# Kernel optimization log

Hardware: AMD Instinct MI355X
Metric: run time of the kernel (lower is better)

## Reference

```python
import jax, jax.numpy as jnp
import numpy as np

N_NODES = 100000
N_EDGES = 640000
D_IN = 128
D_H = 128


def setup_inputs() -> dict:
    key = jax.random.key(0)
    ks = jax.random.split(key, 24)
    def W(k, shp):
        return jax.random.normal(k, shp, dtype=jnp.float32) * 0.05
    inp = {
        "x": jax.random.normal(ks[0], (N_NODES, D_IN), dtype=jnp.float32),
        "src": jax.random.randint(ks[1], (N_EDGES,), 0, N_NODES, dtype=jnp.int32),
        "dst": jax.random.randint(ks[2], (N_EDGES,), 0, N_NODES, dtype=jnp.int32),
        "neg_src": jax.random.randint(ks[3], (N_EDGES,), 0, N_NODES, dtype=jnp.int32),
        "neg_dst": jax.random.randint(ks[4], (N_EDGES,), 0, N_NODES, dtype=jnp.int32),
        # SAGEConv layer 1/2/3: fc_self weight, fc_neigh weight (stored [in,out]), bias
        "Ws1": W(ks[5], (D_IN, D_H)), "Wn1": W(ks[6], (D_IN, D_H)), "b1": jnp.zeros((D_H,), jnp.float32),
        "Ws2": W(ks[7], (D_H, D_H)), "Wn2": W(ks[8], (D_H, D_H)), "b2": jnp.zeros((D_H,), jnp.float32),
        "Ws3": W(ks[9], (D_H, D_H)), "Wn3": W(ks[10], (D_H, D_H)), "b3": jnp.zeros((D_H,), jnp.float32),
        # MLPPredictor: W1 [2h,h], W2 [h,1]
        "Wp1": W(ks[11], (2 * D_H, D_H)), "bp1": jnp.zeros((D_H,), jnp.float32),
        "Wp2": W(ks[12], (D_H, 1)), "bp2": jnp.zeros((1,), jnp.float32),
    }
    return inp


def _sage_mean(x, src, dst, Ws, Wn, b):
    # DGL SAGEConv 'mean': rst = fc_self(h) + fc_neigh(mean_{in-neighbors}(h)) + bias
    n = x.shape[0]
    msum = jax.ops.segment_sum(x[src], dst, num_segments=n)        # [N, d]
    deg = jax.ops.segment_sum(jnp.ones_like(src, dtype=x.dtype), dst, num_segments=n)
    mean = msum / jnp.clip(deg, 1.0)[:, None]                      # zero for isolated nodes
    return x @ Ws + mean @ Wn + b


def _edge_score(h, s, d, Wp1, bp1, Wp2, bp2):
    z = jnp.concatenate([h[s], h[d]], axis=1)                      # [E, 2h]
    return (jax.nn.relu(z @ Wp1 + bp1) @ Wp2 + bp2)[:, 0]          # [E]


def reference(x, src, dst, neg_src, neg_dst,
              Ws1, Wn1, b1, Ws2, Wn2, b2, Ws3, Wn3, b3,
              Wp1, bp1, Wp2, bp2):
    h = _sage_mean(x, src, dst, Ws1, Wn1, b1)
    h = _sage_mean(h, src, dst, Ws2, Wn2, b2)
    h = _sage_mean(h, src, dst, Ws3, Wn3, b3)
    pos = _edge_score(h, src, dst, Wp1, bp1, Wp2, bp2)
    neg = _edge_score(h, neg_src, neg_dst, Wp1, bp1, Wp2, bp2)
    return (pos, neg)
```

## Files before the change

kernel.cpp:

```cpp
#include <hip/hip_runtime.h>

#define N_NODES 100000
#define N_EDGES 640000
#define D 128
#define SCAN_TILE 1024
#define SCAN_BLOCKS ((N_NODES + SCAN_TILE - 1) / SCAN_TILE)

typedef __attribute__((ext_vector_type(8))) short bf16x8;
typedef __attribute__((ext_vector_type(4))) float f32x4;

__device__ __forceinline__ unsigned short f32_to_bf16(float f) {
  union { float f; unsigned int u; } v; v.f = f;
  unsigned int u = v.u;
  unsigned int r = (u + 0x7fffu + ((u >> 16) & 1u)) >> 16;
  return (unsigned short)r;
}
__device__ __forceinline__ float bf16_lo(unsigned int u) { return __uint_as_float(u << 16); }
__device__ __forceinline__ float bf16_hi(unsigned int u) { return __uint_as_float(u & 0xffff0000u); }

__device__ __forceinline__ void acc8(float* a, uint4 r) {
  a[0] += bf16_lo(r.x); a[1] += bf16_hi(r.x);
  a[2] += bf16_lo(r.y); a[3] += bf16_hi(r.y);
  a[4] += bf16_lo(r.z); a[5] += bf16_hi(r.z);
  a[6] += bf16_lo(r.w); a[7] += bf16_hi(r.w);
}

__global__ void zero_i32(int* __restrict__ p, int n) {
  int i = blockIdx.x * blockDim.x + threadIdx.x;
  if (i < n) p[i] = 0;
}

__global__ void f32_to_bf16_vec(const float* __restrict__ in, unsigned short* __restrict__ out, int n4) {
  int i = blockIdx.x * blockDim.x + threadIdx.x;
  if (i < n4) {
    float4 v = ((const float4*)in)[i];
    ushort4 o;
    o.x = f32_to_bf16(v.x); o.y = f32_to_bf16(v.y);
    o.z = f32_to_bf16(v.z); o.w = f32_to_bf16(v.w);
    ((ushort4*)out)[i] = o;
  }
}

__global__ void transpose_w(const float* __restrict__ W0, const float* __restrict__ W1,
                            const float* __restrict__ W2, const float* __restrict__ W3,
                            const float* __restrict__ W4, const float* __restrict__ W5,
                            const float* __restrict__ W6, const float* __restrict__ W7,
                            unsigned short* __restrict__ wt) {
  int id = blockIdx.x * 256 + threadIdx.x;
  int mat = id >> 14;
  int rem = id & 16383;
  int n = rem >> 7, k = rem & 127;
  const float* Wm = mat < 4 ? (mat < 2 ? (mat == 0 ? W0 : W1) : (mat == 2 ? W2 : W3))
                            : (mat < 6 ? (mat == 4 ? W4 : W5) : (mat == 6 ? W6 : W7));
  wt[id] = f32_to_bf16(Wm[k * D + n]);
}

__global__ void hist_kernel(const int* __restrict__ dst, int* __restrict__ deg, int E) {
  int i = blockIdx.x * blockDim.x + threadIdx.x;
  if (i < E) atomicAdd(&deg[dst[i]], 1);
}

__global__ void scan_blocksum(const int* __restrict__ deg, int* __restrict__ partial, int n) {
  __shared__ int lds[256];
  const int tid = threadIdx.x;
  const int base = blockIdx.x * SCAN_TILE + tid * 4;
  int s = 0;
#pragma unroll
  for (int j = 0; j < 4; ++j) {
    int i = base + j;
    if (i < n) s += deg[i];
  }
  lds[tid] = s;
  __syncthreads();
  for (int off = 128; off > 0; off >>= 1) {
    if (tid < off) lds[tid] += lds[tid + off];
    __syncthreads();
  }
  if (tid == 0) partial[blockIdx.x] = lds[0];
}

__global__ void scan_offsets(int* __restrict__ partial, int* __restrict__ row_start, int nb, int n) {
  __shared__ int lds[128];
  const int tid = threadIdx.x;
  int v = (tid < nb) ? partial[tid] : 0;
  lds[tid] = v;
  __syncthreads();
  for (int off = 1; off < 128; off <<= 1) {
    int t = (tid >= off) ? lds[tid - off] : 0;
    __syncthreads();
    lds[tid] += t;
    __syncthreads();
  }
  if (tid < nb) partial[tid] = (tid == 0) ? 0 : lds[tid - 1];
  if (tid == 0) row_start[n] = lds[nb - 1];
}

__global__ void scan_final(const int* __restrict__ deg, const int* __restrict__ partial,
                           int* __restrict__ row_start, int n) {
  __shared__ int lds[256];
  const int tid = threadIdx.x;
  const int base = blockIdx.x * SCAN_TILE + tid * 4;
  int d[4];
  int s = 0;
#pragma unroll
  for (int j = 0; j < 4; ++j) {
    int i = base + j;
    d[j] = (i < n) ? deg[i] : 0;
    s += d[j];
  }
  lds[tid] = s;
  __syncthreads();
  for (int off = 1; off < 256; off <<= 1) {
    int t = (tid >= off) ? lds[tid - off] : 0;
    __syncthreads();
    lds[tid] += t;
    __syncthreads();
  }
  int pre = partial[blockIdx.x] + lds[tid] - s;
#pragma unroll
  for (int j = 0; j < 4; ++j) {
    int i = base + j;
    if (i < n) {
      row_start[i] = pre;
      pre += d[j];
    }
  }
}

__global__ void fill_kernel(const int* __restrict__ src, const int* __restrict__ dst,
                            const int* __restrict__ row_start, int* __restrict__ cursor,
                            int* __restrict__ esrc, int E) {
  int i = blockIdx.x * blockDim.x + threadIdx.x;
  if (i < E) {
    int d = dst[i];
    int pos = atomicAdd(&cursor[d], 1);
    esrc[row_start[d] + pos] = src[i];
  }
}

__global__ __launch_bounds__(256) void gather_mean(
    const unsigned short* __restrict__ hin,
    const int* __restrict__ row_start, const int* __restrict__ esrc,
    unsigned short* __restrict__ mean, int M) {
  const int t = blockIdx.x * blockDim.x + threadIdx.x;
  const int node = t >> 4;
  const int fl = t & 15;
  if (node >= M) return;
  const int s0 = row_start[node], s1 = row_start[node + 1];
  float ac[8] = {0.f, 0.f, 0.f, 0.f, 0.f, 0.f, 0.f, 0.f};
  int e = s0;
  for (; e + 4 <= s1; e += 4) {
    int i0 = esrc[e], i1 = esrc[e + 1], i2 = esrc[e + 2], i3 = esrc[e + 3];
    uint4 r0 = *(const uint4*)(hin + (((size_t)i0) << 7) + fl * 8);
    uint4 r1 = *(const uint4*)(hin + (((size_t)i1) << 7) + fl * 8);
    uint4 r2 = *(const uint4*)(hin + (((size_t)i2) << 7) + fl * 8);
    uint4 r3 = *(const uint4*)(hin + (((size_t)i3) << 7) + fl * 8);
    acc8(ac, r0); acc8(ac, r1); acc8(ac, r2); acc8(ac, r3);
  }
  for (; e < s1; ++e) {
    uint4 r0 = *(const uint4*)(hin + (((size_t)esrc[e]) << 7) + fl * 8);
    acc8(ac, r0);
  }
  const float inv = 1.0f / (float)max(s1 - s0, 1);
#pragma unroll
  for (int k = 0; k < 8; ++k) ac[k] *= inv;
  uint4 o;
  o.x = (unsigned)f32_to_bf16(ac[0]) | ((unsigned)f32_to_bf16(ac[1]) << 16);
  o.y = (unsigned)f32_to_bf16(ac[2]) | ((unsigned)f32_to_bf16(ac[3]) << 16);
  o.z = (unsigned)f32_to_bf16(ac[4]) | ((unsigned)f32_to_bf16(ac[5]) << 16);
  o.w = (unsigned)f32_to_bf16(ac[6]) | ((unsigned)f32_to_bf16(ac[7]) << 16);
  *reinterpret_cast<uint4*>(mean + (((size_t)node) << 7) + fl * 8) = o;
}

template <bool PRED>
__global__ __launch_bounds__(256) void layer_mlp(
    const unsigned short* __restrict__ hin,
    const unsigned short* __restrict__ mean,
    const unsigned short* __restrict__ Wts, const unsigned short* __restrict__ Wtn,
    const float* __restrict__ bias,
    const unsigned short* __restrict__ WtA, const unsigned short* __restrict__ WtB,
    const float* __restrict__ biasA,
    unsigned short* __restrict__ out0, unsigned short* __restrict__ out1, int M) {
  __shared__ unsigned short wl[64][136];
  const int tid = threadIdx.x;
  const int lane = tid & 63;
  const int wave = tid >> 6;
  const int m0 = blockIdx.x * 128;
  const int row = lane & 15;
  const int q = lane >> 4;
  const int mloadA = min(m0 + wave * 16 + row, M - 1);
  const int mloadB = min(m0 + 64 + wave * 16 + row, M - 1);
  const int lrow = wave * 16 + row;

  auto stage64 = [&](const unsigned short* W, int half) {
#pragma unroll
    for (int i = 0; i < 4; ++i) {
      int seg = i * 256 + tid;
      int r = seg >> 4, o = (seg & 15) * 8;
      *reinterpret_cast<bf16x8*>(&wl[r][o]) =
          *reinterpret_cast<const bf16x8*>(W + (size_t)(half * 64 + r) * D + o);
    }
  };
  auto mfma_half = [&](bf16x8* a, f32x4* accp) {
#pragma unroll
    for (int s = 0; s < 4; ++s)
#pragma unroll
      for (int t = 0; t < 4; ++t) {
        bf16x8 b = *reinterpret_cast<const bf16x8*>(&wl[t * 16 + row][s * 32 + q * 8]);
        accp[t] = __builtin_amdgcn_mfma_f32_16x16x32_bf16(a[s], b, accp[t], 0, 0, 0);
      }
  };
  auto epilogue = [&](f32x4* accp, const float* bvec, unsigned short* dst, int base) {
    __syncthreads();
#pragma unroll
    for (int t = 0; t < 8; ++t) {
      const int col = t * 16 + row;
      const float bv = bvec ? bvec[col] : 0.f;
#pragma unroll
      for (int r = 0; r < 4; ++r)
        wl[wave * 16 + q * 4 + r][col] = f32_to_bf16(accp[t][r] + bv);
    }
    __syncthreads();
#pragma unroll
    for (int i = 0; i < 4; ++i) {
      int idx = i * 256 + tid;
      int r2 = idx >> 4;
      int c8 = (idx & 15) * 8;
      int m = base + r2;
      if (m < M)
        *reinterpret_cast<uint4*>(dst + (size_t)m * D + c8) =
            *reinterpret_cast<const uint4*>(&wl[r2][c8]);
    }
  };

  stage64(Wts, 0);
  bf16x8 ahA[4], amA[4], ahB[4], amB[4];
#pragma unroll
  for (int s = 0; s < 4; ++s) {
    ahA[s] = *reinterpret_cast<const bf16x8*>(hin + (size_t)mloadA * D + s * 32 + q * 8);
    amA[s] = *reinterpret_cast<const bf16x8*>(mean + (size_t)mloadA * D + s * 32 + q * 8);
    ahB[s] = *reinterpret_cast<const bf16x8*>(hin + (size_t)mloadB * D + s * 32 + q * 8);
    amB[s] = *reinterpret_cast<const bf16x8*>(mean + (size_t)mloadB * D + s * 32 + q * 8);
  }
  __syncthreads();

  f32x4 accA[8], accB[8];
#pragma unroll
  for (int t = 0; t < 8; ++t) { accA[t] = (f32x4){0.f, 0.f, 0.f, 0.f}; accB[t] = (f32x4){0.f, 0.f, 0.f, 0.f}; }

  mfma_half(ahA, accA); mfma_half(ahB, accB);
  __syncthreads(); stage64(Wts, 1); __syncthreads();
  mfma_half(ahA, accA + 4); mfma_half(ahB, accB + 4);
  __syncthreads(); stage64(Wtn, 0); __syncthreads();
  mfma_half(amA, accA); mfma_half(amB, accB);
  __syncthreads(); stage64(Wtn, 1); __syncthreads();
  mfma_half(amA, accA + 4); mfma_half(amB, accB + 4);

  if (!PRED) {
    epilogue(accA, bias, out0, m0);
    epilogue(accB, bias, out0, m0 + 64);
    return;
  }

  __syncthreads();
  bf16x8 apA[4], apB[4];
#pragma unroll
  for (int t = 0; t < 8; ++t) {
    const int col = t * 16 + row;
    const float bv = bias[col];
#pragma unroll
    for (int r = 0; r < 4; ++r)
      wl[wave * 16 + q * 4 + r][col] = f32_to_bf16(accA[t][r] + bv);
  }
#pragma unroll
  for (int s = 0; s < 4; ++s)
    apA[s] = *reinterpret_cast<const bf16x8*>(&wl[lrow][s * 32 + q * 8]);
#pragma unroll
  for (int t = 0; t < 8; ++t) {
    const int col = t * 16 + row;
    const float bv = bias[col];
#pragma unroll
    for (int r = 0; r < 4; ++r)
      wl[wave * 16 + q * 4 + r][col] = f32_to_bf16(accB[t][r] + bv);
  }
#pragma unroll
  for (int s = 0; s < 4; ++s)
    apB[s] = *reinterpret_cast<const bf16x8*>(&wl[lrow][s * 32 + q * 8]);
  __syncthreads();

  stage64(WtA, 0);
  __syncthreads();
#pragma unroll
  for (int t = 0; t < 8; ++t) { accA[t] = (f32x4){0.f, 0.f, 0.f, 0.f}; accB[t] = (f32x4){0.f, 0.f, 0.f, 0.f}; }
  mfma_half(apA, accA); mfma_half(apB, accB);
  __syncthreads(); stage64(WtA, 1); __syncthreads();
  mfma_half(apA, accA + 4); mfma_half(apB, accB + 4);
  epilogue(accA, biasA, out0, m0);
  epilogue(accB, biasA, out0, m0 + 64);
  __syncthreads();
  stage64(WtB, 0);
  __syncthreads();
#pragma unroll
  for (int t = 0; t < 8; ++t) { accA[t] = (f32x4){0.f, 0.f, 0.f, 0.f}; accB[t] = (f32x4){0.f, 0.f, 0.f, 0.f}; }
  mfma_half(apA, accA); mfma_half(apB, accB);
  __syncthreads(); stage64(WtB, 1); __syncthreads();
  mfma_half(apA, accA + 4); mfma_half(apB, accB + 4);
  epilogue(accA, nullptr, out1, m0);
  epilogue(accB, nullptr, out1, m0 + 64);
}

__device__ __forceinline__ float relu_dot8(uint4 a, uint4 b, float4 w0, float4 w1) {
  return fmaxf(bf16_lo(a.x) + bf16_lo(b.x), 0.f) * w0.x +
         fmaxf(bf16_hi(a.x) + bf16_hi(b.x), 0.f) * w0.y +
         fmaxf(bf16_lo(a.y) + bf16_lo(b.y), 0.f) * w0.z +
         fmaxf(bf16_hi(a.y) + bf16_hi(b.y), 0.f) * w0.w +
         fmaxf(bf16_lo(a.z) + bf16_lo(b.z), 0.f) * w1.x +
         fmaxf(bf16_hi(a.z) + bf16_hi(b.z), 0.f) * w1.y +
         fmaxf(bf16_lo(a.w) + bf16_lo(b.w), 0.f) * w1.z +
         fmaxf(bf16_hi(a.w) + bf16_hi(b.w), 0.f) * w1.w;
}

__global__ __launch_bounds__(256) void edge_score4(
    const unsigned short* __restrict__ A, const unsigned short* __restrict__ B,
    const int* __restrict__ ss, const int* __restrict__ dd,
    const float* __restrict__ Wp2, const float* __restrict__ bp2,
    float* __restrict__ out, int E) {
  const int t = blockIdx.x * blockDim.x + threadIdx.x;
  const int g = t >> 4;
  const int fl = t & 15;
  const int e0 = g * 4;
  if (e0 >= E) return;
  const int4 s4 = *(const int4*)(ss + e0);
  const int4 d4 = *(const int4*)(dd + e0);
  const float4 w0 = *(const float4*)(Wp2 + fl * 8);
  const float4 w1 = *(const float4*)(Wp2 + fl * 8 + 4);
  const size_t fo = (size_t)(fl * 8);

  uint4 a0 = *(const uint4*)(A + (((size_t)s4.x << 7) + fo));
  uint4 b0 = *(const uint4*)(B + (((size_t)d4.x << 7) + fo));
  uint4 a1 = *(const uint4*)(A + (((size_t)s4.y << 7) + fo));
  uint4 b1 = *(const uint4*)(B + (((size_t)d4.y << 7) + fo));
  uint4 a2 = *(const uint4*)(A + (((size_t)s4.z << 7) + fo));
  uint4 b2 = *(const uint4*)(B + (((size_t)d4.z << 7) + fo));
  uint4 a3 = *(const uint4*)(A + (((size_t)s4.w << 7) + fo));
  uint4 b3 = *(const uint4*)(B + (((size_t)d4.w << 7) + fo));

  float p0 = relu_dot8(a0, b0, w0, w1);
  float p1 = relu_dot8(a1, b1, w0, w1);
  float p2 = relu_dot8(a2, b2, w0, w1);
  float p3 = relu_dot8(a3, b3, w0, w1);

  p0 += __shfl_xor(p0, 1); p1 += __shfl_xor(p1, 1); p2 += __shfl_xor(p2, 1); p3 += __shfl_xor(p3, 1);
  p0 += __shfl_xor(p0, 2); p1 += __shfl_xor(p1, 2); p2 += __shfl_xor(p2, 2); p3 += __shfl_xor(p3, 2);
  p0 += __shfl_xor(p0, 4); p1 += __shfl_xor(p1, 4); p2 += __shfl_xor(p2, 4); p3 += __shfl_xor(p3, 4);
  p0 += __shfl_xor(p0, 8); p1 += __shfl_xor(p1, 8); p2 += __shfl_xor(p2, 8); p3 += __shfl_xor(p3, 8);

  if (fl == 0) {
    const float bv = bp2[0];
    *reinterpret_cast<float4*>(out + e0) = make_float4(p0 + bv, p1 + bv, p2 + bv, p3 + bv);
  }
}

extern "C" void kernel_launch(void* const* d_in, const int* in_sizes, int n_in,
                              void* d_out, int out_size, void* d_ws, size_t ws_size,
                              hipStream_t stream) {
  const float* x = (const float*)d_in[0];
  const int* src = (const int*)d_in[1];
  const int* dst = (const int*)d_in[2];
  const int* nsrc = (const int*)d_in[3];
  const int* ndst = (const int*)d_in[4];
  const float* Ws1 = (const float*)d_in[5];
  const float* Wn1 = (const float*)d_in[6];
  const float* b1 = (const float*)d_in[7];
  const float* Ws2 = (const float*)d_in[8];
  const float* Wn2 = (const float*)d_in[9];
  const float* b2 = (const float*)d_in[10];
  const float* Ws3 = (const float*)d_in[11];
  const float* Wn3 = (const float*)d_in[12];
  const float* b3 = (const float*)d_in[13];
  const float* Wp1 = (const float*)d_in[14];
  const float* bp1 = (const float*)d_in[15];
  const float* Wp2 = (const float*)d_in[16];
  const float* bp2 = (const float*)d_in[17];
  float* out = (float*)d_out;

  char* ws = (char*)d_ws;
  size_t off = 0;
  auto alloc = [&](size_t bytes) -> void* {
    void* p = ws + off;
    off += (bytes + 255) & ~(size_t)255;
    return p;
  };
  const size_t NODE_F32 = sizeof(float) * (size_t)N_NODES * D;
  char* region0 = (char*)alloc(NODE_F32);
  char* region1 = (char*)alloc(NODE_F32);
  unsigned short* meanb = (unsigned short*)alloc(sizeof(unsigned short) * (size_t)N_NODES * D);
  int* row_start = (int*)alloc(sizeof(int) * (N_NODES + 1));
  int* deg = (int*)alloc(sizeof(int) * N_NODES * 2);
  int* cursor = deg + N_NODES;
  int* esrc = (int*)alloc(sizeof(int) * N_EDGES);
  int* partial = (int*)alloc(sizeof(int) * 128);
  unsigned short* wt = (unsigned short*)alloc(sizeof(unsigned short) * 8 * D * D);
  (void)ws_size;

  unsigned short* xb = (unsigned short*)region0;
  unsigned short* hA = (unsigned short*)region1;
  unsigned short* hB = hA + (size_t)N_NODES * D;
  unsigned short* Ab = xb;
  unsigned short* Bb = xb + (size_t)N_NODES * D;

  f32_to_bf16_vec<<<(N_NODES * D / 4 + 255) / 256, 256, 0, stream>>>(x, xb, N_NODES * D / 4);
  transpose_w<<<512, 256, 0, stream>>>(Ws1, Wn1, Ws2, Wn2, Ws3, Wn3, Wp1, Wp1 + D * D, wt);

  zero_i32<<<(2 * N_NODES + 255) / 256, 256, 0, stream>>>(deg, 2 * N_NODES);
  hist_kernel<<<(N_EDGES + 255) / 256, 256, 0, stream>>>(dst, deg, N_EDGES);
  scan_blocksum<<<SCAN_BLOCKS, 256, 0, stream>>>(deg, partial, N_NODES);
  scan_offsets<<<1, 128, 0, stream>>>(partial, row_start, SCAN_BLOCKS, N_NODES);
  scan_final<<<SCAN_BLOCKS, 256, 0, stream>>>(deg, partial, row_start, N_NODES);
  fill_kernel<<<(N_EDGES + 255) / 256, 256, 0, stream>>>(src, dst, row_start, cursor, esrc, N_EDGES);

  const int gatherBlocks = (N_NODES * 16 + 255) / 256;
  const int mlpBlocks = (N_NODES + 127) / 128;
  const int edgeBlocks = (N_EDGES / 4 * 16) / 256;

  gather_mean<<<gatherBlocks, 256, 0, stream>>>(xb, row_start, esrc, meanb, N_NODES);
  layer_mlp<false><<<mlpBlocks, 256, 0, stream>>>(
      xb, meanb, wt, wt + 16384, b1, nullptr, nullptr, nullptr, hA, nullptr, N_NODES);
  gather_mean<<<gatherBlocks, 256, 0, stream>>>(hA, row_start, esrc, meanb, N_NODES);
  layer_mlp<false><<<mlpBlocks, 256, 0, stream>>>(
      hA, meanb, wt + 2 * 16384, wt + 3 * 16384, b2, nullptr, nullptr, nullptr, hB, nullptr, N_NODES);
  gather_mean<<<gatherBlocks, 256, 0, stream>>>(hB, row_start, esrc, meanb, N_NODES);
  layer_mlp<true><<<mlpBlocks, 256, 0, stream>>>(
      hB, meanb, wt + 4 * 16384, wt + 5 * 16384, b3, wt + 6 * 16384, wt + 7 * 16384, bp1,
      Ab, Bb, N_NODES);
  edge_score4<<<edgeBlocks, 256, 0, stream>>>(Ab, Bb, src, dst, Wp2, bp2, out, N_EDGES);
  edge_score4<<<edgeBlocks, 256, 0, stream>>>(Ab, Bb, nsrc, ndst, Wp2, bp2, out + N_EDGES, N_EDGES);
}
```

Before: 460.3 us.

## Use persistent weight-resident MLP kernel for layers 1-2 and merge edge scoring launches

```diff
diff --git a/kernel.cpp b/kernel.cpp
--- a/kernel.cpp
+++ b/kernel.cpp
@@ -170,6 +170,90 @@
   o.z = (unsigned)f32_to_bf16(ac[4]) | ((unsigned)f32_to_bf16(ac[5]) << 16);
   o.w = (unsigned)f32_to_bf16(ac[6]) | ((unsigned)f32_to_bf16(ac[7]) << 16);
   *reinterpret_cast<uint4*>(mean + (((size_t)node) << 7) + fl * 8) = o;
+}
+
+__global__ __launch_bounds__(512, 1) void layer_persist(
+    const unsigned short* __restrict__ hin,
+    const unsigned short* __restrict__ mean,
+    const unsigned short* __restrict__ Wts, const unsigned short* __restrict__ Wtn,
+    const float* __restrict__ bias,
+    unsigned short* __restrict__ out0, int M, int C) {
+  __shared__ unsigned short ws[128][136];
+  __shared__ unsigned short wn[128][136];
+  __shared__ unsigned short et[8][16][136];
+  const int tid = threadIdx.x;
+  const int wave = tid >> 6;
+  const int lane = tid & 63;
+  const int row = lane & 15;
+  const int q = lane >> 4;
+
+#pragma unroll
+  for (int i = 0; i < 4; ++i) {
+    int seg = i * 512 + tid;
+    int r = seg >> 4, o = (seg & 15) * 8;
+    *reinterpret_cast<bf16x8*>(&ws[r][o]) = *reinterpret_cast<const bf16x8*>(Wts + r * D + o);
+    *reinterpret_cast<bf16x8*>(&wn[r][o]) = *reinterpret_cast<const bf16x8*>(Wtn + r * D + o);
+  }
+  float bv[8];
+#pragma unroll
+  for (int t = 0; t < 8; ++t) bv[t] = bias[t * 16 + row];
+  __syncthreads();
+
+  auto ldfr = [&](const unsigned short* p, int mload, bf16x8* f) {
+#pragma unroll
+    for (int s = 0; s < 4; ++s)
+      f[s] = *reinterpret_cast<const bf16x8*>(p + (size_t)mload * D + s * 32 + q * 8);
+  };
+
+  int c = blockIdx.x * 8 + wave;
+  if (c >= C) return;
+  bf16x8 ah[4], am[4], nh[4], nm[4];
+  ldfr(hin, min(c * 16 + row, M - 1), ah);
+  ldfr(mean, min(c * 16 + row, M - 1), am);
+
+  while (true) {
+    const int cn = c + 2048;
+    if (cn < C) {
+      ldfr(hin, min(cn * 16 + row, M - 1), nh);
+      ldfr(mean, min(cn * 16 + row, M - 1), nm);
+    }
+    f32x4 acc[8];
+#pragma unroll
+    for (int t = 0; t < 8; ++t) acc[t] = (f32x4){0.f, 0.f, 0.f, 0.f};
+#pragma unroll
+    for (int s = 0; s < 4; ++s)
+#pragma unroll
+      for (int t = 0; t < 8; ++t)
+        acc[t] = __builtin_amdgcn_mfma_f32_16x16x32_bf16(
+            ah[s], *reinterpret_cast<const bf16x8*>(&ws[t * 16 + row][s * 32 + q * 8]), acc[t], 0, 0, 0);
+#pragma unroll
+    for (int s = 0; s < 4; ++s)
+#pragma unroll
+      for (int t = 0; t < 8; ++t)
+        acc[t] = __builtin_amdgcn_mfma_f32_16x16x32_bf16(
+            am[s], *reinterpret_cast<const bf16x8*>(&wn[t * 16 + row][s * 32 + q * 8]), acc[t], 0, 0, 0);
+#pragma unroll
+    for (int t = 0; t < 8; ++t) {
+      const int col = t * 16 + row;
+#pragma unroll
+      for (int r2 = 0; r2 < 4; ++r2)
+        et[wave][q * 4 + r2][col] = f32_to_bf16(acc[t][r2] + bv[t]);
+    }
+    const int m16 = c * 16;
+#pragma unroll
+    for (int j = 0; j < 4; ++j) {
+      int k = j * 64 + lane;
+      int r2 = k >> 4, c8 = (k & 15) * 8;
+      int m = m16 + r2;
+      if (m < M)
+        *reinterpret_cast<uint4*>(out0 + (size_t)m * D + c8) =
+            *reinterpret_cast<const uint4*>(&et[wave][r2][c8]);
+    }
+    if (cn >= C) break;
+    c = cn;
+#pragma unroll
+    for (int s = 0; s < 4; ++s) { ah[s] = nh[s]; am[s] = nm[s]; }
+  }
 }
 
 template <bool PRED>
@@ -322,14 +406,21 @@
 
 __global__ __launch_bounds__(256) void edge_score4(
     const unsigned short* __restrict__ A, const unsigned short* __restrict__ B,
-    const int* __restrict__ ss, const int* __restrict__ dd,
+    const int* __restrict__ ps, const int* __restrict__ pd,
+    const int* __restrict__ ns, const int* __restrict__ nd,
     const float* __restrict__ Wp2, const float* __restrict__ bp2,
     float* __restrict__ out, int E) {
   const int t = blockIdx.x * blockDim.x + threadIdx.x;
-  const int g = t >> 4;
+  const int g2 = t >> 4;
   const int fl = t & 15;
+  const int g = g2 >> 1;
   const int e0 = g * 4;
   if (e0 >= E) return;
+  const bool neg = (g2 & 1) != 0;
+  const int* ss = neg ? ns : ps;
+  const int* dd = neg ? nd : pd;
+  float* op = neg ? out + E : out;
+
   const int4 s4 = *(const int4*)(ss + e0);
   const int4 d4 = *(const int4*)(dd + e0);
   const float4 w0 = *(const float4*)(Wp2 + fl * 8);
@@ -357,7 +448,7 @@
 
   if (fl == 0) {
     const float bv = bp2[0];
-    *reinterpret_cast<float4*>(out + e0) = make_float4(p0 + bv, p1 + bv, p2 + bv, p3 + bv);
+    *reinterpret_cast<float4*>(op + e0) = make_float4(p0 + bv, p1 + bv, p2 + bv, p3 + bv);
   }
 }
 
@@ -420,19 +511,19 @@
   fill_kernel<<<(N_EDGES + 255) / 256, 256, 0, stream>>>(src, dst, row_start, cursor, esrc, N_EDGES);
 
   const int gatherBlocks = (N_NODES * 16 + 255) / 256;
-  const int mlpBlocks = (N_NODES + 127) / 128;
-  const int edgeBlocks = (N_EDGES / 4 * 16) / 256;
+  const int CHUNKS = (N_NODES + 15) / 16;
+  const int predBlocks = (N_NODES + 127) / 128;
+  const int edgeBlocks = (2 * (N_EDGES / 4) * 16) / 256;
 
   gather_mean<<<gatherBlocks, 256, 0, stream>>>(xb, row_start, esrc, meanb, N_NODES);
-  layer_mlp<false><<<mlpBlocks, 256, 0, stream>>>(
-      xb, meanb, wt, wt + 16384, b1, nullptr, nullptr, nullptr, hA, nullptr, N_NODES);
+  layer_persist<<<256, 512, 0, stream>>>(
+      xb, meanb, wt, wt + 16384, b1, hA, N_NODES, CHUNKS);
   gather_mean<<<gatherBlocks, 256, 0, stream>>>(hA, row_start, esrc, meanb, N_NODES);
-  layer_mlp<false><<<mlpBlocks, 256, 0, stream>>>(
-      hA, meanb, wt + 2 * 16384, wt + 3 * 16384, b2, nullptr, nullptr, nullptr, hB, nullptr, N_NODES);
+  layer_persist<<<256, 512, 0, stream>>>(
+      hA, meanb, wt + 2 * 16384, wt + 3 * 16384, b2, hB, N_NODES, CHUNKS);
   gather_mean<<<gatherBlocks, 256, 0, stream>>>(hB, row_start, esrc, meanb, N_NODES);
-  layer_mlp<true><<<mlpBlocks, 256, 0, stream>>>(
+  layer_mlp<true><<<predBlocks, 256, 0, stream>>>(
       hB, meanb, wt + 4 * 16384, wt + 5 * 16384, b3, wt + 6 * 16384, wt + 7 * 16384, bp1,
       Ab, Bb, N_NODES);
-  edge_score4<<<edgeBlocks, 256, 0, stream>>>(Ab, Bb, src, dst, Wp2, bp2, out, N_EDGES);
-  edge_score4<<<edgeBlocks, 256, 0, stream>>>(Ab, Bb, nsrc, ndst, Wp2, bp2, out + N_EDGES, N_EDGES);
-}
+  edge_score4<<<edgeBlocks, 256, 0, stream>>>(Ab, Bb, src, dst, nsrc, ndst, Wp2, bp2, out, N_EDGES);
+}
```

Result: slower. 519.1 us (+12.8%).
